# Optimization experiments

Measured on AMD Instinct MI355X. Metric: run time of the kernel, lower is better.

## Reference

```python
import jax, jax.numpy as jnp
import numpy as np

N = 4096      # num nodes/docs (<= max_compare=5000, so no random subsampling)
IN = 768      # input feature dim
OUT = 512     # projector output dim
TEM = 0.5     # temperature
BN_EPS = 1e-5
NORM_EPS = 1e-12


def setup_inputs() -> dict:
    key = jax.random.key(0)
    ks = jax.random.split(key, 5)
    doc0 = jax.random.normal(ks[0], (N, IN), dtype=jnp.float32)
    doc1 = jax.random.normal(ks[1], (N, IN), dtype=jnp.float32)
    doc2 = jax.random.normal(ks[2], (N, IN), dtype=jnp.float32)
    # 6 freshly-initialized projectors (one per view per pair, as in the torch forward)
    W1s = jax.random.normal(ks[3], (6, IN, OUT), dtype=jnp.float32) * 0.05
    b1s = jnp.zeros((6, OUT), dtype=jnp.float32)
    gammas = jnp.ones((6, OUT), dtype=jnp.float32)
    betas = jnp.zeros((6, OUT), dtype=jnp.float32)
    W2s = jax.random.normal(ks[4], (6, OUT, OUT), dtype=jnp.float32) * 0.05
    b2s = jnp.zeros((6, OUT), dtype=jnp.float32)
    return {"doc0": doc0, "doc1": doc1, "doc2": doc2,
            "W1s": W1s, "b1s": b1s, "gammas": gammas, "betas": betas,
            "W2s": W2s, "b2s": b2s}


def _projector(x, W1, b1, g, b, W2, b2):
    # Linear -> BatchNorm1d (training-mode batch stats) -> ReLU -> Linear
    h = x @ W1 + b1
    mu = h.mean(axis=0)
    var = h.var(axis=0)  # biased, matching torch BN normalization
    h = (h - mu) * jax.lax.rsqrt(var + BN_EPS) * g + b
    h = jax.nn.relu(h)
    return h @ W2 + b2


def _l2norm(x):
    n = jnp.sqrt(jnp.sum(x * x, axis=1, keepdims=True))
    return x / jnp.maximum(n, NORM_EPS)


def _pair_loss(a, b):
    # a, b: [N, OUT], already L2-normalized.
    # Full-matrix form of the chunked batch_loss (mathematically identical).
    refl = jnp.exp((a @ a.T) / TEM)      # [N, N]
    between = jnp.exp((a @ b.T) / TEM)   # [N, N]
    pos = jnp.diagonal(between)
    denom = refl.sum(axis=1) + between.sum(axis=1) - jnp.diagonal(refl)
    return -jnp.log(pos / denom)


def reference(doc0, doc1, doc2, W1s, b1s, gammas, betas, W2s, b2s):
    docs = [doc0, doc1, doc2]
    pairs = [(0, 1), (0, 2), (1, 2)]
    total = jnp.float32(0.0)
    k = 0
    for (i, j) in pairs:
        o1 = _l2norm(_projector(docs[i], W1s[k], b1s[k], gammas[k], betas[k], W2s[k], b2s[k]))
        k += 1
        o2 = _l2norm(_projector(docs[j], W1s[k], b1s[k], gammas[k], betas[k], W2s[k], b2s[k]))
        k += 1
        l = 0.5 * (_pair_loss(o1, o2) + _pair_loss(o2, o1))
        total = total + l.mean()
    return total / 3.0
```

## Files before the change

kernel.cpp:

```cpp
#include <hip/hip_runtime.h>
#include <hip/hip_bf16.h>
#include <hip/hip_fp8.h>

#define N_ROWS 4096
#define IN_DIM 768
#define OUT_DIM 512


using bf16x8 = __attribute__((ext_vector_type(8))) short;
using f32x4  = __attribute__((ext_vector_type(4))) float;
using i64    = long;
using i64x2  = __attribute__((ext_vector_type(2))) long;

__device__ __constant__ int c_docmap[6] = {0, 1, 0, 2, 1, 2};

__device__ inline unsigned short f2bf(float f) {
    __hip_bfloat16 h = __float2bfloat16(f);
    return reinterpret_cast<unsigned short&>(h);
}
__device__ inline float bf2f(unsigned short u) {
    return __uint_as_float((unsigned int)u << 16);
}
__device__ inline unsigned char f2fp8(float f) {
    __hip_fp8_e4m3 t(f);
    return t.__x;
}
__device__ inline uint4 pack8bf(const float* v) {
    uint4 o;
    unsigned short* p = (unsigned short*)&o;
#pragma unroll
    for (int j = 0; j < 8; ++j) p[j] = f2bf(v[j]);
    return o;
}

__global__ __launch_bounds__(256) void prep(
    const float* __restrict__ d0, const float* __restrict__ d1,
    const float* __restrict__ d2, const float* __restrict__ W1s,
    const float* __restrict__ W2s, unsigned short* __restrict__ Xb,
    unsigned short* __restrict__ W1t, unsigned short* __restrict__ W2t,
    char* __restrict__ zbase) {
    int wunit = blockIdx.x * 4 + (threadIdx.x >> 6);
    int lane = threadIdx.x & 63;
    int lane15 = lane & 15, quad = lane >> 4;
    if (wunit < 18432) {
        int d = wunit / 6144, u = wunit % 6144;
        int gt = u / 24, kf = u % 24;
        const float* src = (d == 0) ? d0 : ((d == 1) ? d1 : d2);
        const float* s = src + (size_t)(gt * 16 + lane15) * IN_DIM + kf * 32 + quad * 8;
        float4 a = *(const float4*)s, b = *(const float4*)(s + 4);
        float v[8] = {a.x, a.y, a.z, a.w, b.x, b.y, b.z, b.w};
        *(uint4*)(Xb + (size_t)d * N_ROWS * IN_DIM + (size_t)u * 512 + lane * 8) = pack8bf(v);
    } else if (wunit < 23040) {
        int v0 = wunit - 18432;
        int z = v0 / 768, u = v0 % 768;
        int gt = u / 24, kf = u % 24;
        int n = gt * 16 + lane15;
        int k0 = kf * 32 + quad * 8;
        const float* W = W1s + (size_t)z * IN_DIM * OUT_DIM;
        float v[8];
#pragma unroll
        for (int j = 0; j < 8; ++j) v[j] = W[(size_t)(k0 + j) * OUT_DIM + n];
        *(uint4*)(W1t + (size_t)z * OUT_DIM * IN_DIM + (size_t)u * 512 + lane * 8) = pack8bf(v);
    } else if (wunit < 26112) {
        int v0 = wunit - 23040;
        int z = v0 / 512, u = v0 % 512;
        int gt = u / 16, kf = u % 16;
        int n = gt * 16 + lane15;
        int k0 = kf * 32 + quad * 8;
        const float* W = W2s + (size_t)z * OUT_DIM * OUT_DIM;
        float v[8];
#pragma unroll
        for (int j = 0; j < 8; ++j) v[j] = W[(size_t)(k0 + j) * OUT_DIM + n];
        *(uint4*)(W2t + (size_t)z * OUT_DIM * OUT_DIM + (size_t)u * 512 + lane * 8) = pack8bf(v);
    } else {
        size_t b = (size_t)(wunit - 26112) * 1024 + (size_t)lane * 16;
        if (b < (size_t)(24576 + 98304 + 98304))
            *(float4*)(zbase + b) = (float4){0.f, 0.f, 0.f, 0.f};
    }
}

__global__ __launch_bounds__(512) void gemm1_bn(
    const unsigned short* __restrict__ Xb, const unsigned short* __restrict__ W1t,
    const float* __restrict__ biasAll, float* __restrict__ H,
    float* __restrict__ stats) {
    const int NKF = IN_DIM / 32;
    int z = blockIdx.z;
    const unsigned short* A = Xb + (size_t)c_docmap[z] * N_ROWS * IN_DIM;
    const unsigned short* B = W1t + (size_t)z * OUT_DIM * IN_DIM;
    const float* bz = biasAll + (size_t)z * OUT_DIM;
    float* C = H + (size_t)z * N_ROWS * OUT_DIM;

    int m0 = blockIdx.y * 256, n0 = blockIdx.x * 128;
    int tid = threadIdx.x;
    int wave = tid >> 6, lane = tid & 63;
    int lane15 = lane & 15, quad = lane >> 4;
    int wrow = (wave >> 1) * 64, wcol = (wave & 1) * 64;

    const unsigned short* Ca = A + (size_t)((m0 + wrow) >> 4) * NKF * 512 + (size_t)lane * 8;
    const unsigned short* Cb = B + (size_t)((n0 + wcol) >> 4) * NKF * 512 + (size_t)lane * 8;

    f32x4 acc[4][4];
#pragma unroll
    for (int mt = 0; mt < 4; ++mt)
#pragma unroll
        for (int nt = 0; nt < 4; ++nt)
            acc[mt][nt] = (f32x4){0.f, 0.f, 0.f, 0.f};

    bf16x8 aC[4], bC[4], aN[4], bN[4];
#pragma unroll
    for (int t = 0; t < 4; ++t) {
        aC[t] = *(const bf16x8*)(Ca + (size_t)t * NKF * 512);
        bC[t] = *(const bf16x8*)(Cb + (size_t)t * NKF * 512);
    }
#pragma unroll
    for (int kf = 0; kf < NKF; ++kf) {
        if (kf < NKF - 1) {
#pragma unroll
            for (int t = 0; t < 4; ++t) {
                aN[t] = *(const bf16x8*)(Ca + (size_t)t * NKF * 512 + (kf + 1) * 512);
                bN[t] = *(const bf16x8*)(Cb + (size_t)t * NKF * 512 + (kf + 1) * 512);
            }
        }
#pragma unroll
        for (int mt = 0; mt < 4; ++mt)
#pragma unroll
            for (int nt = 0; nt < 4; ++nt)
                acc[mt][nt] = __builtin_amdgcn_mfma_f32_16x16x32_bf16(aC[mt], bC[nt], acc[mt][nt], 0, 0, 0);
#pragma unroll
        for (int t = 0; t < 4; ++t) { aC[t] = aN[t]; bC[t] = bN[t]; }
    }

    float s1[4] = {0.f, 0.f, 0.f, 0.f}, s2[4] = {0.f, 0.f, 0.f, 0.f};
#pragma unroll
    for (int nt = 0; nt < 4; ++nt) {
        int col = n0 + wcol + nt * 16 + lane15;
        float bv = bz[col];
#pragma unroll
        for (int mt = 0; mt < 4; ++mt)
#pragma unroll
            for (int r = 0; r < 4; ++r) {
                int row = m0 + wrow + mt * 16 + quad * 4 + r;
                float v = acc[mt][nt][r] + bv;
                C[(size_t)row * OUT_DIM + col] = v;
                s1[nt] += v; s2[nt] += v * v;
            }
    }
#pragma unroll
    for (int nt = 0; nt < 4; ++nt) {
        float a = s1[nt], b = s2[nt];
        a += __shfl_xor(a, 16); a += __shfl_xor(a, 32);
        b += __shfl_xor(b, 16); b += __shfl_xor(b, 32);
        if (quad == 0) {
            int col = n0 + wcol + nt * 16 + lane15;
            atomicAdd(&stats[((size_t)z * OUT_DIM + col) * 2 + 0], a);
            atomicAdd(&stats[((size_t)z * OUT_DIM + col) * 2 + 1], b);
        }
    }
}

__global__ __launch_bounds__(256) void bn_apply(
    const float* __restrict__ H, unsigned short* __restrict__ Hb,
    const float* __restrict__ stats, const float* __restrict__ gammas,
    const float* __restrict__ betas) {
    int wunit = blockIdx.x * 4 + (threadIdx.x >> 6);
    if (wunit >= 24576) return;
    int lane = threadIdx.x & 63;
    int lane15 = lane & 15, quad = lane >> 4;
    int z = wunit / 4096, u = wunit % 4096;
    int gt = u / 16, kf = u % 16;
    int row = gt * 16 + lane15;
    int k = kf * 32 + quad * 8;
    const float* Hp = H + ((size_t)z * N_ROWS + row) * OUT_DIM + k;
    float4 a = *(const float4*)Hp, b = *(const float4*)(Hp + 4);
    float hv[8] = {a.x, a.y, a.z, a.w, b.x, b.y, b.z, b.w};
    float v[8];
#pragma unroll
    for (int j = 0; j < 8; ++j) {
        size_t sc = (size_t)z * OUT_DIM + k + j;
        float mu = stats[sc * 2 + 0] * (1.f / N_ROWS);
        float var = stats[sc * 2 + 1] * (1.f / N_ROWS) - mu * mu;
        float t = (hv[j] - mu) * rsqrtf(var + 1e-5f) * gammas[sc] + betas[sc];
        v[j] = fmaxf(t, 0.f);
    }
    *(uint4*)(Hb + (size_t)z * N_ROWS * OUT_DIM + (size_t)u * 512 + lane * 8) = pack8bf(v);
}

__global__ __launch_bounds__(512) void gemm2_norm(
    const unsigned short* __restrict__ Hb, const unsigned short* __restrict__ W2t,
    const float* __restrict__ biasAll, unsigned short* __restrict__ O,
    float* __restrict__ rowsumsq) {
    const int NKF = OUT_DIM / 32;
    int z = blockIdx.z;
    const unsigned short* A = Hb + (size_t)z * N_ROWS * OUT_DIM;
    const unsigned short* B = W2t + (size_t)z * OUT_DIM * OUT_DIM;
    const float* bz = biasAll + (size_t)z * OUT_DIM;
    unsigned short* C = O + (size_t)z * N_ROWS * OUT_DIM;
    float* rq = rowsumsq + (size_t)z * N_ROWS;

    int m0 = blockIdx.y * 256, n0 = blockIdx.x * 128;
    int tid = threadIdx.x;
    int wave = tid >> 6, lane = tid & 63;
    int lane15 = lane & 15, quad = lane >> 4;
    int wrow = (wave >> 1) * 64, wcol = (wave & 1) * 64;

    const unsigned short* Ca = A + (size_t)((m0 + wrow) >> 4) * NKF * 512 + (size_t)lane * 8;
    const unsigned short* Cb = B + (size_t)((n0 + wcol) >> 4) * NKF * 512 + (size_t)lane * 8;

    f32x4 acc[4][4];
#pragma unroll
    for (int mt = 0; mt < 4; ++mt)
#pragma unroll
        for (int nt = 0; nt < 4; ++nt)
            acc[mt][nt] = (f32x4){0.f, 0.f, 0.f, 0.f};

    bf16x8 aC[4], bC[4], aN[4], bN[4];
#pragma unroll
    for (int t = 0; t < 4; ++t) {
        aC[t] = *(const bf16x8*)(Ca + (size_t)t * NKF * 512);
        bC[t] = *(const bf16x8*)(Cb + (size_t)t * NKF * 512);
    }
#pragma unroll
    for (int kf = 0; kf < NKF; ++kf) {
        if (kf < NKF - 1) {
#pragma unroll
            for (int t = 0; t < 4; ++t) {
                aN[t] = *(const bf16x8*)(Ca + (size_t)t * NKF * 512 + (kf + 1) * 512);
                bN[t] = *(const bf16x8*)(Cb + (size_t)t * NKF * 512 + (kf + 1) * 512);
            }
        }
#pragma unroll
        for (int mt = 0; mt < 4; ++mt)
#pragma unroll
            for (int nt = 0; nt < 4; ++nt)
                acc[mt][nt] = __builtin_amdgcn_mfma_f32_16x16x32_bf16(aC[mt], bC[nt], acc[mt][nt], 0, 0, 0);
#pragma unroll
        for (int t = 0; t < 4; ++t) { aC[t] = aN[t]; bC[t] = bN[t]; }
    }

    float rs[16];
#pragma unroll
    for (int j = 0; j < 16; ++j) rs[j] = 0.f;
#pragma unroll
    for (int nt = 0; nt < 4; ++nt) {
        int col = n0 + wcol + nt * 16 + lane15;
        float bv = bz[col];
#pragma unroll
        for (int mt = 0; mt < 4; ++mt)
#pragma unroll
            for (int r = 0; r < 4; ++r) {
                int row = m0 + wrow + mt * 16 + quad * 4 + r;
                float v = acc[mt][nt][r] + bv;
                C[(size_t)row * OUT_DIM + col] = f2bf(v);
                rs[mt * 4 + r] += v * v;
            }
    }
#pragma unroll
    for (int j = 0; j < 16; ++j) {
        float v = rs[j];
        v += __shfl_xor(v, 1); v += __shfl_xor(v, 2);
        v += __shfl_xor(v, 4); v += __shfl_xor(v, 8);
        if (lane15 == 0) {
            int row = m0 + wrow + (j >> 2) * 16 + quad * 4 + (j & 3);
            atomicAdd(&rq[row], v);
        }
    }
}

__global__ __launch_bounds__(256) void l2norm_fp8(const unsigned short* __restrict__ O,
                                                  const float* __restrict__ rowsumsq,
                                                  unsigned char* __restrict__ A) {
    int gt = blockIdx.x;
    int wave = threadIdx.x >> 6, lane = threadIdx.x & 63;
    int lane15 = lane & 15, quad = lane >> 4;
    int row = gt * 16 + lane15;
    float sc = 1.f / fmaxf(sqrtf(rowsumsq[row]), 1e-12f);
    const unsigned short* Op = O + (size_t)row * OUT_DIM + quad * 8;
#pragma unroll
    for (int t = 0; t < 2; ++t) {
        int kh = wave * 2 + t;
        unsigned long long pk[2];
#pragma unroll
        for (int half = 0; half < 2; ++half) {
            int kf = kh * 2 + half;
            uint4 u = *(const uint4*)(Op + kf * 32);
            unsigned int w[4] = {u.x, u.y, u.z, u.w};
            unsigned long long v = 0;
#pragma unroll
            for (int j = 0; j < 8; ++j) {
                unsigned short us = (j & 1) ? (unsigned short)(w[j >> 1] >> 16)
                                            : (unsigned short)(w[j >> 1] & 0xffff);
                v |= (unsigned long long)f2fp8(bf2f(us) * sc) << (8 * j);
            }
            pk[half] = v;
        }
        i64x2 st; st[0] = (i64)pk[0]; st[1] = (i64)pk[1];
        *(i64x2*)(A + ((size_t)(gt * 8 + kh) * 64 + lane) * 16) = st;
    }
}

__global__ __launch_bounds__(512) void gram_kernel(const unsigned char* __restrict__ Abase,
                                                   float* __restrict__ rowsum,
                                                   float* __restrict__ crossdot) {
    int px = blockIdx.x;
    int logical = (px & 7) * 396 + (px >> 3);
    int p = logical / 1056;
    int t0 = logical - p * 1056;
    const unsigned char* Cm = Abase + (size_t)p * 2 * N_ROWS * OUT_DIM;

    int I = 0;
    while (t0 >= 64 - 2 * I) { t0 -= 64 - 2 * I; ++I; }
    int J = 2 * I + t0;
    int m0 = I * 256, n0 = J * 128;

    int tid = threadIdx.x;
    int wave = tid >> 6, lane = tid & 63;
    int lane15 = lane & 15, quad = lane >> 4;
    int wrow = (wave >> 1) * 64, wcol = (wave & 1) * 64;

    const unsigned char* Ca = Cm + (size_t)((m0 + wrow) >> 4) * 8192 + (size_t)lane * 16;
    const unsigned char* Cb = Cm + (size_t)((n0 + wcol) >> 4) * 8192 + (size_t)lane * 16;

    f32x4 acc[4][4];
#pragma unroll
    for (int mt = 0; mt < 4; ++mt)
#pragma unroll
        for (int nt = 0; nt < 4; ++nt)
            acc[mt][nt] = (f32x4){0.f, 0.f, 0.f, 0.f};

    i64x2 aC[4], bC[4], aN[4], bN[4];
#pragma unroll
    for (int t = 0; t < 4; ++t) {
        aC[t] = *(const i64x2*)(Ca + (size_t)t * 8192);
        bC[t] = *(const i64x2*)(Cb + (size_t)t * 8192);
    }
#pragma unroll
    for (int kh = 0; kh < 8; ++kh) {
        if (kh < 7) {
#pragma unroll
            for (int t = 0; t < 4; ++t) {
                aN[t] = *(const i64x2*)(Ca + (size_t)t * 8192 + (kh + 1) * 1024);
                bN[t] = *(const i64x2*)(Cb + (size_t)t * 8192 + (kh + 1) * 1024);
            }
        }
#pragma unroll
        for (int half = 0; half < 2; ++half)
#pragma unroll
            for (int mt = 0; mt < 4; ++mt)
#pragma unroll
                for (int nt = 0; nt < 4; ++nt)
                    acc[mt][nt] = __builtin_amdgcn_mfma_f32_16x16x32_fp8_fp8(
                        aC[mt][half], bC[nt][half], acc[mt][nt], 0, 0, 0);
#pragma unroll
        for (int t = 0; t < 4; ++t) { aC[t] = aN[t]; bC[t] = bN[t]; }
    }

    float* cdp = crossdot + (size_t)p * 2 * N_ROWS;
    float* rp  = rowsum  + (size_t)p * 2 * N_ROWS;

    float rs[16];
    float cs[4] = {0.f, 0.f, 0.f, 0.f};
#pragma unroll
    for (int j = 0; j < 16; ++j) rs[j] = 0.f;

    if (J >= 2 * I + 2) {
#pragma unroll
        for (int mt = 0; mt < 4; ++mt)
#pragma unroll
            for (int nt = 0; nt < 4; ++nt)
#pragma unroll
                for (int r = 0; r < 4; ++r) {
                    float e = __expf(2.f * acc[mt][nt][r]);
                    rs[mt * 4 + r] += e;
                    cs[nt] += e;
                }
        if (J >= 32 && ((J - 32) >> 1) == I) {
#pragma unroll
            for (int mt = 0; mt < 4; ++mt)
#pragma unroll
                for (int nt = 0; nt < 4; ++nt) {
                    int gcol = n0 + wcol + nt * 16 + lane15;
#pragma unroll
                    for (int r = 0; r < 4; ++r) {
                        int grow = m0 + wrow + mt * 16 + quad * 4 + r;
                        if (gcol == grow + N_ROWS) {
                            float s = acc[mt][nt][r];
                            cdp[grow] = s;
                            cdp[gcol] = s;
                        }
                    }
                }
        }
    } else {
#pragma unroll
        for (int mt = 0; mt < 4; ++mt)
#pragma unroll
            for (int nt = 0; nt < 4; ++nt) {
                int gcol = n0 + wcol + nt * 16 + lane15;
#pragma unroll
                for (int r = 0; r < 4; ++r) {
                    int grow = m0 + wrow + mt * 16 + quad * 4 + r;
                    if (grow < gcol) {
                        float e = __expf(2.f * acc[mt][nt][r]);
                        rs[mt * 4 + r] += e;
                        cs[nt] += e;
                    }
                }
            }
    }

#pragma unroll
    for (int j = 0; j < 16; ++j) {
        float v = rs[j];
        v += __shfl_xor(v, 1); v += __shfl_xor(v, 2);
        v += __shfl_xor(v, 4); v += __shfl_xor(v, 8);
        rs[j] = v;
    }
    if (lane15 == 0) {
#pragma unroll
        for (int j = 0; j < 16; ++j) {
            int grow = m0 + wrow + (j >> 2) * 16 + quad * 4 + (j & 3);
            atomicAdd(&rp[grow], rs[j]);
        }
    }
#pragma unroll
    for (int n = 0; n < 4; ++n) {
        float v = cs[n];
        v += __shfl_xor(v, 16); v += __shfl_xor(v, 32);
        cs[n] = v;
    }
    if (quad == 0) {
#pragma unroll
        for (int n = 0; n < 4; ++n) {
            int gcol = n0 + wcol + n * 16 + lane15;
            atomicAdd(&rp[gcol], cs[n]);
        }
    }
}

__global__ void loss_kernel(const float* __restrict__ rowsum,
                            const float* __restrict__ crossdot, float* __restrict__ out) {
    __shared__ float red[256];
    float acc = 0.f;
    for (int i = threadIdx.x; i < 3 * 2 * N_ROWS; i += 256) {
        acc += logf(rowsum[i]) - 2.f * crossdot[i];
    }
    red[threadIdx.x] = acc;
    __syncthreads();
    for (int s = 128; s > 0; s >>= 1) {
        if (threadIdx.x < s) red[threadIdx.x] += red[threadIdx.x + s];
        __syncthreads();
    }
    if (threadIdx.x == 0) out[0] = red[0] * (1.f / 24576.f);
}

extern "C" void kernel_launch(void* const* d_in, const int* in_sizes, int n_in,
                              void* d_out, int out_size, void* d_ws, size_t ws_size,
                              hipStream_t stream) {
    const float* doc0   = (const float*)d_in[0];
    const float* doc1   = (const float*)d_in[1];
    const float* doc2   = (const float*)d_in[2];
    const float* W1s    = (const float*)d_in[3];
    const float* b1s    = (const float*)d_in[4];
    const float* gammas = (const float*)d_in[5];
    const float* betas  = (const float*)d_in[6];
    const float* W2s    = (const float*)d_in[7];
    const float* b2s    = (const float*)d_in[8];
    float* out = (float*)d_out;

    char* base = (char*)d_ws;
    size_t off = 0;
    auto alloc = [&](size_t bytes) -> char* {
        char* r = base + off;
        off += (bytes + 255) & ~(size_t)255;
        return r;
    };

    unsigned short* Xb   = (unsigned short*)alloc((size_t)3 * N_ROWS * IN_DIM * 2);
    unsigned short* W1t  = (unsigned short*)alloc((size_t)6 * OUT_DIM * IN_DIM * 2);
    unsigned short* W2t  = (unsigned short*)alloc((size_t)6 * OUT_DIM * OUT_DIM * 2);
    float*          H    = (float*)         alloc((size_t)6 * N_ROWS * OUT_DIM * 4);
    unsigned short* Hb   = (unsigned short*)alloc((size_t)6 * N_ROWS * OUT_DIM * 2);
    unsigned char*  Abuf = (unsigned char*)Xb;
    unsigned short* O    = (unsigned short*)H;
    char* zbase = alloc(24576 + 98304 + 98304);
    float* stats    = (float*)zbase;
    float* rowsumsq = (float*)(zbase + 24576);
    float* rowsum   = (float*)(zbase + 24576 + 98304);
    float* cdot     = (float*)alloc((size_t)3 * 2 * N_ROWS * 4);

    if (ws_size < off) return;

    prep<<<6582, 256, 0, stream>>>(doc0, doc1, doc2, W1s, W2s, Xb, W1t, W2t, zbase);

    gemm1_bn<<<dim3(OUT_DIM / 128, N_ROWS / 256, 6), 512, 0, stream>>>(Xb, W1t, b1s, H, stats);

    bn_apply<<<6144, 256, 0, stream>>>(H, Hb, stats, gammas, betas);

    gemm2_norm<<<dim3(OUT_DIM / 128, N_ROWS / 256, 6), 512, 0, stream>>>(Hb, W2t, b2s, O, rowsumsq);

    l2norm_fp8<<<1536, 256, 0, stream>>>(O, rowsumsq, Abuf);

    gram_kernel<<<3168, 512, 0, stream>>>(Abuf, rowsum, cdot);

    loss_kernel<<<1, 256, 0, stream>>>(rowsum, cdot, out);
}
```

Baseline: 339.3 us.

## Fuse BN-apply into GEMM2 prologue and L2-norm/FP8 pack into its epilogue

Drops the separate bn_apply and l2norm_fp8 kernels. GEMM2 now reads the fp32 H directly and applies BN scale/shift plus ReLU and bf16 conversion in registers, using per-column coefficients from a small bn_coef kernel. Each block covers all 512 output columns for 64 rows, so the row L2 norm is reduced in shared memory and the result is written straight to the packed fp8 buffer. This removes the rowsumsq atomics, the bf16 intermediate and two launches. In exchange, GEMM2 loads fp32 A data (twice the bytes) and both GEMMs shrink to 384-block grids, which may leave compute units underused.

Measured after the change: 362.8 us. +6.9%, slower.

```diff
diff --git a/kernel.cpp b/kernel.cpp
--- a/kernel.cpp
+++ b/kernel.cpp
@@ -17,9 +17,6 @@
 __device__ inline unsigned short f2bf(float f) {
     __hip_bfloat16 h = __float2bfloat16(f);
     return reinterpret_cast<unsigned short&>(h);
-}
-__device__ inline float bf2f(unsigned short u) {
-    return __uint_as_float((unsigned int)u << 16);
 }
 __device__ inline unsigned char f2fp8(float f) {
     __hip_fp8_e4m3 t(f);
@@ -74,7 +71,7 @@
         *(uint4*)(W2t + (size_t)z * OUT_DIM * OUT_DIM + (size_t)u * 512 + lane * 8) = pack8bf(v);
     } else {
         size_t b = (size_t)(wunit - 26112) * 1024 + (size_t)lane * 16;
-        if (b < (size_t)(24576 + 98304 + 98304))
+        if (b < (size_t)(24576 + 98304))
             *(float4*)(zbase + b) = (float4){0.f, 0.f, 0.f, 0.f};
     }
 }
@@ -84,20 +81,20 @@
     const float* __restrict__ biasAll, float* __restrict__ H,
     float* __restrict__ stats) {
     const int NKF = IN_DIM / 32;
-    int z = blockIdx.z;
+    int z = blockIdx.y;
+    int m0 = blockIdx.x * 64;
     const unsigned short* A = Xb + (size_t)c_docmap[z] * N_ROWS * IN_DIM;
     const unsigned short* B = W1t + (size_t)z * OUT_DIM * IN_DIM;
     const float* bz = biasAll + (size_t)z * OUT_DIM;
     float* C = H + (size_t)z * N_ROWS * OUT_DIM;
 
-    int m0 = blockIdx.y * 256, n0 = blockIdx.x * 128;
     int tid = threadIdx.x;
     int wave = tid >> 6, lane = tid & 63;
     int lane15 = lane & 15, quad = lane >> 4;
-    int wrow = (wave >> 1) * 64, wcol = (wave & 1) * 64;
-
-    const unsigned short* Ca = A + (size_t)((m0 + wrow) >> 4) * NKF * 512 + (size_t)lane * 8;
-    const unsigned short* Cb = B + (size_t)((n0 + wcol) >> 4) * NKF * 512 + (size_t)lane * 8;
+    int wcol = wave * 64;
+
+    const unsigned short* Ca = A + (size_t)(m0 >> 4) * NKF * 512 + (size_t)lane * 8;
+    const unsigned short* Cb = B + (size_t)(wave * 4) * NKF * 512 + (size_t)lane * 8;
 
     f32x4 acc[4][4];
 #pragma unroll
@@ -133,13 +130,13 @@
     float s1[4] = {0.f, 0.f, 0.f, 0.f}, s2[4] = {0.f, 0.f, 0.f, 0.f};
 #pragma unroll
     for (int nt = 0; nt < 4; ++nt) {
-        int col = n0 + wcol + nt * 16 + lane15;
+        int col = wcol + nt * 16 + lane15;
         float bv = bz[col];
 #pragma unroll
         for (int mt = 0; mt < 4; ++mt)
 #pragma unroll
             for (int r = 0; r < 4; ++r) {
-                int row = m0 + wrow + mt * 16 + quad * 4 + r;
+                int row = m0 + mt * 16 + quad * 4 + r;
                 float v = acc[mt][nt][r] + bv;
                 C[(size_t)row * OUT_DIM + col] = v;
                 s1[nt] += v; s2[nt] += v * v;
@@ -151,60 +148,49 @@
         a += __shfl_xor(a, 16); a += __shfl_xor(a, 32);
         b += __shfl_xor(b, 16); b += __shfl_xor(b, 32);
         if (quad == 0) {
-            int col = n0 + wcol + nt * 16 + lane15;
+            int col = wcol + nt * 16 + lane15;
             atomicAdd(&stats[((size_t)z * OUT_DIM + col) * 2 + 0], a);
             atomicAdd(&stats[((size_t)z * OUT_DIM + col) * 2 + 1], b);
         }
     }
 }
 
-__global__ __launch_bounds__(256) void bn_apply(
-    const float* __restrict__ H, unsigned short* __restrict__ Hb,
-    const float* __restrict__ stats, const float* __restrict__ gammas,
-    const float* __restrict__ betas) {
-    int wunit = blockIdx.x * 4 + (threadIdx.x >> 6);
-    if (wunit >= 24576) return;
-    int lane = threadIdx.x & 63;
-    int lane15 = lane & 15, quad = lane >> 4;
-    int z = wunit / 4096, u = wunit % 4096;
-    int gt = u / 16, kf = u % 16;
-    int row = gt * 16 + lane15;
-    int k = kf * 32 + quad * 8;
-    const float* Hp = H + ((size_t)z * N_ROWS + row) * OUT_DIM + k;
-    float4 a = *(const float4*)Hp, b = *(const float4*)(Hp + 4);
-    float hv[8] = {a.x, a.y, a.z, a.w, b.x, b.y, b.z, b.w};
-    float v[8];
-#pragma unroll
-    for (int j = 0; j < 8; ++j) {
-        size_t sc = (size_t)z * OUT_DIM + k + j;
-        float mu = stats[sc * 2 + 0] * (1.f / N_ROWS);
-        float var = stats[sc * 2 + 1] * (1.f / N_ROWS) - mu * mu;
-        float t = (hv[j] - mu) * rsqrtf(var + 1e-5f) * gammas[sc] + betas[sc];
-        v[j] = fmaxf(t, 0.f);
-    }
-    *(uint4*)(Hb + (size_t)z * N_ROWS * OUT_DIM + (size_t)u * 512 + lane * 8) = pack8bf(v);
-}
-
-__global__ __launch_bounds__(512) void gemm2_norm(
-    const unsigned short* __restrict__ Hb, const unsigned short* __restrict__ W2t,
-    const float* __restrict__ biasAll, unsigned short* __restrict__ O,
-    float* __restrict__ rowsumsq) {
+__global__ void bn_coef(const float* __restrict__ stats, const float* __restrict__ gammas,
+                        const float* __restrict__ betas, float* __restrict__ bnc) {
+    int i = blockIdx.x * 256 + threadIdx.x;
+    if (i >= 6 * OUT_DIM) return;
+    int z = i >> 9, c = i & 511;
+    float mu = stats[(size_t)i * 2 + 0] * (1.f / N_ROWS);
+    float var = stats[(size_t)i * 2 + 1] * (1.f / N_ROWS) - mu * mu;
+    float sc = gammas[i] * rsqrtf(var + 1e-5f);
+    bnc[(size_t)z * 1024 + c] = sc;
+    bnc[(size_t)z * 1024 + 512 + c] = betas[i] - mu * sc;
+}
+
+__global__ __launch_bounds__(512) void gemm2_fused(
+    const float* __restrict__ H, const unsigned short* __restrict__ W2t,
+    const float* __restrict__ bnc, const float* __restrict__ biasAll,
+    unsigned char* __restrict__ Abuf) {
     const int NKF = OUT_DIM / 32;
-    int z = blockIdx.z;
-    const unsigned short* A = Hb + (size_t)z * N_ROWS * OUT_DIM;
+    int z = blockIdx.y;
+    int m0 = blockIdx.x * 64;
+    const float* A = H + (size_t)z * N_ROWS * OUT_DIM;
     const unsigned short* B = W2t + (size_t)z * OUT_DIM * OUT_DIM;
+    const float* scp = bnc + (size_t)z * 1024;
+    const float* shp = bnc + (size_t)z * 1024 + 512;
     const float* bz = biasAll + (size_t)z * OUT_DIM;
-    unsigned short* C = O + (size_t)z * N_ROWS * OUT_DIM;
-    float* rq = rowsumsq + (size_t)z * N_ROWS;
-
-    int m0 = blockIdx.y * 256, n0 = blockIdx.x * 128;
+    unsigned char* Az = Abuf + (size_t)z * N_ROWS * OUT_DIM;
+
     int tid = threadIdx.x;
     int wave = tid >> 6, lane = tid & 63;
     int lane15 = lane & 15, quad = lane >> 4;
-    int wrow = (wave >> 1) * 64, wcol = (wave & 1) * 64;
-
-    const unsigned short* Ca = A + (size_t)((m0 + wrow) >> 4) * NKF * 512 + (size_t)lane * 8;
-    const unsigned short* Cb = B + (size_t)((n0 + wcol) >> 4) * NKF * 512 + (size_t)lane * 8;
+    int wcol = wave * 64;
+
+    const float* Ap[4];
+#pragma unroll
+    for (int mt = 0; mt < 4; ++mt)
+        Ap[mt] = A + (size_t)(m0 + mt * 16 + lane15) * OUT_DIM + quad * 8;
+    const unsigned short* Cb = B + (size_t)(wave * 4) * NKF * 512 + (size_t)lane * 8;
 
     f32x4 acc[4][4];
 #pragma unroll
@@ -213,44 +199,68 @@
         for (int nt = 0; nt < 4; ++nt)
             acc[mt][nt] = (f32x4){0.f, 0.f, 0.f, 0.f};
 
-    bf16x8 aC[4], bC[4], aN[4], bN[4];
+    float4 aR0[4], aR1[4], nR0[4], nR1[4];
+    bf16x8 bC[4], bN[4];
 #pragma unroll
     for (int t = 0; t < 4; ++t) {
-        aC[t] = *(const bf16x8*)(Ca + (size_t)t * NKF * 512);
+        aR0[t] = *(const float4*)(Ap[t]);
+        aR1[t] = *(const float4*)(Ap[t] + 4);
         bC[t] = *(const bf16x8*)(Cb + (size_t)t * NKF * 512);
     }
+
 #pragma unroll
     for (int kf = 0; kf < NKF; ++kf) {
         if (kf < NKF - 1) {
 #pragma unroll
             for (int t = 0; t < 4; ++t) {
-                aN[t] = *(const bf16x8*)(Ca + (size_t)t * NKF * 512 + (kf + 1) * 512);
+                nR0[t] = *(const float4*)(Ap[t] + (kf + 1) * 32);
+                nR1[t] = *(const float4*)(Ap[t] + (kf + 1) * 32 + 4);
                 bN[t] = *(const bf16x8*)(Cb + (size_t)t * NKF * 512 + (kf + 1) * 512);
             }
         }
+        int k0 = kf * 32 + quad * 8;
+        float4 sc0 = *(const float4*)(scp + k0), sc1 = *(const float4*)(scp + k0 + 4);
+        float4 sh0 = *(const float4*)(shp + k0), sh1 = *(const float4*)(shp + k0 + 4);
+        bf16x8 aF[4];
+#pragma unroll
+        for (int mt = 0; mt < 4; ++mt) {
+            float v[8];
+            v[0] = fmaxf(fmaf(aR0[mt].x, sc0.x, sh0.x), 0.f);
+            v[1] = fmaxf(fmaf(aR0[mt].y, sc0.y, sh0.y), 0.f);
+            v[2] = fmaxf(fmaf(aR0[mt].z, sc0.z, sh0.z), 0.f);
+            v[3] = fmaxf(fmaf(aR0[mt].w, sc0.w, sh0.w), 0.f);
+            v[4] = fmaxf(fmaf(aR1[mt].x, sc1.x, sh1.x), 0.f);
+            v[5] = fmaxf(fmaf(aR1[mt].y, sc1.y, sh1.y), 0.f);
+            v[6] = fmaxf(fmaf(aR1[mt].z, sc1.z, sh1.z), 0.f);
+            v[7] = fmaxf(fmaf(aR1[mt].w, sc1.w, sh1.w), 0.f);
+            uint4 pk = pack8bf(v);
+            aF[mt] = reinterpret_cast<bf16x8&>(pk);
+        }
 #pragma unroll
         for (int mt = 0; mt < 4; ++mt)
 #pragma unroll
             for (int nt = 0; nt < 4; ++nt)
-                acc[mt][nt] = __builtin_amdgcn_mfma_f32_16x16x32_bf16(aC[mt], bC[nt], acc[mt][nt], 0, 0, 0);
-#pragma unroll
-        for (int t = 0; t < 4; ++t) { aC[t] = aN[t]; bC[t] = bN[t]; }
-    }
+                acc[mt][nt] = __builtin_amdgcn_mfma_f32_16x16x32_bf16(aF[mt], bC[nt], acc[mt][nt], 0, 0, 0);
+#pragma unroll
+        for (int t = 0; t < 4; ++t) { aR0[t] = nR0[t]; aR1[t] = nR1[t]; bC[t] = bN[t]; }
+    }
+
+    __shared__ float part[8][64];
+    __shared__ float scf[64];
+    __shared__ __attribute__((aligned(16))) unsigned char T[64 * 520];
 
     float rs[16];
 #pragma unroll
     for (int j = 0; j < 16; ++j) rs[j] = 0.f;
 #pragma unroll
     for (int nt = 0; nt < 4; ++nt) {
-        int col = n0 + wcol + nt * 16 + lane15;
-        float bv = bz[col];
+        float bv = bz[wcol + nt * 16 + lane15];
 #pragma unroll
         for (int mt = 0; mt < 4; ++mt)
 #pragma unroll
             for (int r = 0; r < 4; ++r) {
-                int row = m0 + wrow + mt * 16 + quad * 4 + r;
                 float v = acc[mt][nt][r] + bv;
-                C[(size_t)row * OUT_DIM + col] = f2bf(v);
+                acc[mt][nt][r] = v;
                 rs[mt * 4 + r] += v * v;
             }
     }
@@ -259,42 +269,40 @@
         float v = rs[j];
         v += __shfl_xor(v, 1); v += __shfl_xor(v, 2);
         v += __shfl_xor(v, 4); v += __shfl_xor(v, 8);
-        if (lane15 == 0) {
-            int row = m0 + wrow + (j >> 2) * 16 + quad * 4 + (j & 3);
-            atomicAdd(&rq[row], v);
-        }
-    }
-}
-
-__global__ __launch_bounds__(256) void l2norm_fp8(const unsigned short* __restrict__ O,
-                                                  const float* __restrict__ rowsumsq,
-                                                  unsigned char* __restrict__ A) {
-    int gt = blockIdx.x;
-    int wave = threadIdx.x >> 6, lane = threadIdx.x & 63;
-    int lane15 = lane & 15, quad = lane >> 4;
-    int row = gt * 16 + lane15;
-    float sc = 1.f / fmaxf(sqrtf(rowsumsq[row]), 1e-12f);
-    const unsigned short* Op = O + (size_t)row * OUT_DIM + quad * 8;
-#pragma unroll
-    for (int t = 0; t < 2; ++t) {
-        int kh = wave * 2 + t;
-        unsigned long long pk[2];
-#pragma unroll
-        for (int half = 0; half < 2; ++half) {
-            int kf = kh * 2 + half;
-            uint4 u = *(const uint4*)(Op + kf * 32);
-            unsigned int w[4] = {u.x, u.y, u.z, u.w};
-            unsigned long long v = 0;
-#pragma unroll
-            for (int j = 0; j < 8; ++j) {
-                unsigned short us = (j & 1) ? (unsigned short)(w[j >> 1] >> 16)
-                                            : (unsigned short)(w[j >> 1] & 0xffff);
-                v |= (unsigned long long)f2fp8(bf2f(us) * sc) << (8 * j);
-            }
-            pk[half] = v;
-        }
-        i64x2 st; st[0] = (i64)pk[0]; st[1] = (i64)pk[1];
-        *(i64x2*)(A + ((size_t)(gt * 8 + kh) * 64 + lane) * 16) = st;
+        rs[j] = v;
+    }
+    if (lane15 == 0) {
+#pragma unroll
+        for (int j = 0; j < 16; ++j)
+            part[wave][(j >> 2) * 16 + quad * 4 + (j & 3)] = rs[j];
+    }
+    __syncthreads();
+    if (tid < 64) {
+        float ss = 0.f;
+#pragma unroll
+        for (int w = 0; w < 8; ++w) ss += part[w][tid];
+        scf[tid] = 1.f / fmaxf(sqrtf(ss), 1e-12f);
+    }
+    __syncthreads();
+#pragma unroll
+    for (int mt = 0; mt < 4; ++mt)
+#pragma unroll
+        for (int r = 0; r < 4; ++r) {
+            int row = mt * 16 + quad * 4 + r;
+            float s = scf[row];
+#pragma unroll
+            for (int nt = 0; nt < 4; ++nt)
+                T[row * 520 + wcol + nt * 16 + lane15] = f2fp8(acc[mt][nt][r] * s);
+        }
+    __syncthreads();
+#pragma unroll
+    for (int gt = 0; gt < 4; ++gt) {
+        int row = gt * 16 + lane15;
+        i64 lo = *(const i64*)(T + row * 520 + (2 * wave) * 32 + quad * 8);
+        i64 hi = *(const i64*)(T + row * 520 + (2 * wave + 1) * 32 + quad * 8);
+        i64x2 st; st[0] = lo; st[1] = hi;
+        int gtg = (m0 >> 4) + gt;
+        *(i64x2*)(Az + ((size_t)(gtg * 8 + wave) * 64 + lane) * 16) = st;
     }
 }
 
@@ -479,26 +487,22 @@
     unsigned short* W1t  = (unsigned short*)alloc((size_t)6 * OUT_DIM * IN_DIM * 2);
     unsigned short* W2t  = (unsigned short*)alloc((size_t)6 * OUT_DIM * OUT_DIM * 2);
     float*          H    = (float*)         alloc((size_t)6 * N_ROWS * OUT_DIM * 4);
-    unsigned short* Hb   = (unsigned short*)alloc((size_t)6 * N_ROWS * OUT_DIM * 2);
     unsigned char*  Abuf = (unsigned char*)Xb;
-    unsigned short* O    = (unsigned short*)H;
-    char* zbase = alloc(24576 + 98304 + 98304);
-    float* stats    = (float*)zbase;
-    float* rowsumsq = (float*)(zbase + 24576);
-    float* rowsum   = (float*)(zbase + 24576 + 98304);
-    float* cdot     = (float*)alloc((size_t)3 * 2 * N_ROWS * 4);
+    char* zbase = alloc(24576 + 98304);
+    float* stats  = (float*)zbase;
+    float* rowsum = (float*)(zbase + 24576);
+    float* bnc    = (float*)alloc((size_t)6 * 1024 * 4);
+    float* cdot   = (float*)alloc((size_t)3 * 2 * N_ROWS * 4);
 
     if (ws_size < off) return;
 
-    prep<<<6582, 256, 0, stream>>>(doc0, doc1, doc2, W1s, W2s, Xb, W1t, W2t, zbase);
-
-    gemm1_bn<<<dim3(OUT_DIM / 128, N_ROWS / 256, 6), 512, 0, stream>>>(Xb, W1t, b1s, H, stats);
-
-    bn_apply<<<6144, 256, 0, stream>>>(H, Hb, stats, gammas, betas);
-
-    gemm2_norm<<<dim3(OUT_DIM / 128, N_ROWS / 256, 6), 512, 0, stream>>>(Hb, W2t, b2s, O, rowsumsq);
-
-    l2norm_fp8<<<1536, 256, 0, stream>>>(O, rowsumsq, Abuf);
+    prep<<<6558, 256, 0, stream>>>(doc0, doc1, doc2, W1s, W2s, Xb, W1t, W2t, zbase);
+
+    gemm1_bn<<<dim3(64, 6), 512, 0, stream>>>(Xb, W1t, b1s, H, stats);
+
+    bn_coef<<<12, 256, 0, stream>>>(stats, gammas, betas, bnc);
+
+    gemm2_fused<<<dim3(64, 6), 512, 0, stream>>>(H, W2t, bnc, b2s, Abuf);
 
     gram_kernel<<<3168, 512, 0, stream>>>(Abuf, rowsum, cdot);
 
```
